# Optimization experiments

Hardware: AMD Instinct MI355X
Metric: run time of the kernel (lower is better)

## Reference

```python
import jax, jax.numpy as jnp
import numpy as np

B, C, H, W, HEADS = 8, 256, 64, 64, 4
EPS = 1e-5  # torch InstanceNorm2d default eps


def conv1x1(x, w):
    # w: [out_c, in_c]; x: [b, in_c, h, w]
    return jnp.einsum('oc,bchw->bohw', w, x)


def maxpool2(x):
    b, c, h, w = x.shape
    return x.reshape(b, c, h // 2, 2, w // 2, 2).max(axis=(3, 5))


def inorm_affine(x, g, b):
    # InstanceNorm2d(affine=True): normalize per (batch, channel) over H,W
    m = jnp.mean(x, axis=(2, 3), keepdims=True)
    v = jnp.mean((x - m) ** 2, axis=(2, 3), keepdims=True)
    return (x - m) * jax.lax.rsqrt(v + EPS) * g[None, :, None, None] + b[None, :, None, None]


def setup_inputs() -> dict:
    key = jax.random.key(0)
    ks = jax.random.split(key, 12)
    s = 1.0 / np.sqrt(C)  # fan-in style scaling for 1x1 conv weights
    return {
        'x': jax.random.normal(ks[0], (B, C, H, W), jnp.float32),
        'theta_w': jax.random.normal(ks[1], (C, C), jnp.float32) * s,
        'phi_w': jax.random.normal(ks[2], (C, C), jnp.float32) * s,
        'g_w': jax.random.normal(ks[3], (C // 2, C), jnp.float32) * s,
        'o_w': jax.random.normal(ks[4], (C, C // 2), jnp.float32) * np.sqrt(2.0 / C),
        'nt_w': 1.0 + 0.1 * jax.random.normal(ks[5], (C,), jnp.float32),
        'nt_b': 0.1 * jax.random.normal(ks[6], (C,), jnp.float32),
        'np_w': 1.0 + 0.1 * jax.random.normal(ks[7], (C,), jnp.float32),
        'np_b': 0.1 * jax.random.normal(ks[8], (C,), jnp.float32),
        'ng_w': 1.0 + 0.1 * jax.random.normal(ks[9], (C // 2,), jnp.float32),
        'ng_b': 0.1 * jax.random.normal(ks[10], (C // 2,), jnp.float32),
        'gamma': jnp.float32(0.5),
    }


def reference(x, theta_w, phi_w, g_w, o_w, nt_w, nt_b, np_w, np_b, ng_w, ng_b, gamma):
    b, c, h, w = x.shape
    n = h * w            # query length
    m = n // 4           # key/value length after 2x2 maxpool
    theta = inorm_affine(conv1x1(x, theta_w), nt_w, nt_b)
    phi = inorm_affine(maxpool2(conv1x1(x, phi_w)), np_w, np_b)
    g = inorm_affine(maxpool2(conv1x1(x, g_w)), ng_w, ng_b)
    # custom head layout: channel dim split as (C//heads, heads), head dim INNER
    theta_ = theta.reshape(b, c // HEADS, HEADS, n)
    phi_ = phi.reshape(b, c // HEADS, HEADS, m)
    g_ = g.reshape(b, (c // 2) // HEADS, HEADS, m)
    beta = jax.nn.softmax(jnp.einsum('bchi,bchj->bhij', theta_, phi_), axis=-1)
    o = jnp.einsum('bchj,bhij->bchi', g_, beta).reshape(b, c // 2, h, w)
    o = conv1x1(o, o_w)
    return gamma * o + x
```

## Files before the change

### kernel.cpp

```cpp
#include <hip/hip_runtime.h>
#include <hip/hip_bf16.h>
#include <math.h>

typedef float f32x4 __attribute__((ext_vector_type(4)));
typedef float f32x16 __attribute__((ext_vector_type(16)));
typedef __bf16 b16x8 __attribute__((ext_vector_type(8)));
typedef __bf16 b16x4 __attribute__((ext_vector_type(4)));
typedef unsigned int u32x2 __attribute__((ext_vector_type(2)));
typedef unsigned int u32x4 __attribute__((ext_vector_type(4)));

#define L2E 1.44269504088896340736f

__global__ void prep_weights(const float* tw, const float* pw, const float* gw,
                             const float* ow, __bf16* Wp, __bf16* OWp) {
    int idx = blockIdx.x * 256 + threadIdx.x;
    if (idx < 640 * 256) {
        int m = idx >> 8, k = idx & 255;
        float v;
        if (m < 256)      { int o = ((m & 63) << 2) + (m >> 6);            v = tw[o * 256 + k]; }
        else if (m < 512) { int mm = m - 256; int o = ((mm & 63) << 2) + (mm >> 6); v = pw[o * 256 + k]; }
        else              { int mm = m - 512; int o = ((mm & 31) << 2) + (mm >> 5); v = gw[o * 256 + k]; }
        Wp[idx] = (__bf16)v;
    } else {
        int j = idx - 640 * 256;
        if (j < 256 * 128) {
            int m = j >> 7, c = j & 127;
            int o = ((c & 31) << 2) + (c >> 5);
            OWp[j] = (__bf16)ow[m * 128 + o];
        }
    }
}

__global__ void transpose_x(const float* x, __bf16* xt) {
    __shared__ float tile[32][33];
    int b = blockIdx.z, c0 = blockIdx.y * 32, p0 = blockIdx.x * 32;
    int tx = threadIdx.x & 31, ty = threadIdx.x >> 5;
#pragma unroll
    for (int i = 0; i < 4; i++) {
        int cy = ty + i * 8;
        tile[cy][tx] = x[((size_t)(b * 256 + c0 + cy)) * 4096 + p0 + tx];
    }
    __syncthreads();
#pragma unroll
    for (int i = 0; i < 4; i++) {
        int py = ty + i * 8;
        xt[((size_t)b * 4096 + p0 + py) * 256 + c0 + tx] = (__bf16)tile[tx][py];
    }
}

__global__ __launch_bounds__(256) void conv_gemm(const __bf16* __restrict__ Wp,
                                                 const __bf16* __restrict__ xt,
                                                 __bf16* theta_t, __bf16* phi_t, __bf16* g_t) {
    int b = blockIdx.z, mt = blockIdx.y, nt = blockIdx.x;
    __shared__ __bf16 Al[128 * 40];
    __shared__ __bf16 Bl[128 * 40];
    int tid = threadIdx.x, l = tid & 63, w = tid >> 6;
    int wm = w >> 1, wn = w & 1, lr = l & 15, lg = l >> 4;
    f32x4 acc[4][4];
#pragma unroll
    for (int i = 0; i < 4; i++)
#pragma unroll
        for (int j = 0; j < 4; j++)
#pragma unroll
            for (int r = 0; r < 4; r++) acc[i][j][r] = 0.f;
    const __bf16* Ag = Wp + (size_t)mt * 128 * 256;
    const __bf16* Bg = xt + ((size_t)b * 4096 + nt * 128) * 256;
    int srow = tid >> 2, scol = (tid & 3) * 8;
    b16x8 aR[2], bR[2];
#pragma unroll
    for (int hh = 0; hh < 2; hh++) {
        int r = srow + hh * 64;
        aR[hh] = *(const b16x8*)&Ag[(size_t)r * 256 + scol];
        bR[hh] = *(const b16x8*)&Bg[(size_t)r * 256 + scol];
    }
    for (int k0 = 0; k0 < 256; k0 += 32) {
        if (k0) __syncthreads();
#pragma unroll
        for (int hh = 0; hh < 2; hh++) {
            int r = srow + hh * 64;
            *(b16x8*)&Al[r * 40 + scol] = aR[hh];
            *(b16x8*)&Bl[r * 40 + scol] = bR[hh];
        }
        __syncthreads();
        if (k0 < 224) {
#pragma unroll
            for (int hh = 0; hh < 2; hh++) {
                int r = srow + hh * 64;
                aR[hh] = *(const b16x8*)&Ag[(size_t)r * 256 + k0 + 32 + scol];
                bR[hh] = *(const b16x8*)&Bg[(size_t)r * 256 + k0 + 32 + scol];
            }
        }
        int ko = lg * 8;
        b16x8 af[4], bfr[4];
#pragma unroll
        for (int i = 0; i < 4; i++) af[i]  = *(b16x8*)&Al[(wm * 64 + i * 16 + lr) * 40 + ko];
#pragma unroll
        for (int i = 0; i < 4; i++) bfr[i] = *(b16x8*)&Bl[(wn * 64 + i * 16 + lr) * 40 + ko];
#pragma unroll
        for (int i = 0; i < 4; i++)
#pragma unroll
            for (int j = 0; j < 4; j++)
                acc[i][j] = __builtin_amdgcn_mfma_f32_16x16x32_bf16(af[i], bfr[j], acc[i][j], 0, 0, 0);
    }
    int rbase = lg * 4;
#pragma unroll
    for (int i = 0; i < 4; i++) {
        int m = mt * 128 + wm * 64 + i * 16 + rbase;
#pragma unroll
        for (int j = 0; j < 4; j++) {
            int p = nt * 128 + wn * 64 + j * 16 + lr;
            b16x4 v;
#pragma unroll
            for (int r = 0; r < 4; r++) v[r] = (__bf16)acc[i][j][r];
            if (m < 256)      *(b16x4*)&theta_t[((size_t)b * 4096 + p) * 256 + m] = v;
            else if (m < 512) *(b16x4*)&phi_t[((size_t)b * 4096 + p) * 256 + (m - 256)] = v;
            else              *(b16x4*)&g_t[((size_t)b * 4096 + p) * 128 + (m - 512)] = v;
        }
    }
}

__global__ __launch_bounds__(256) void theta_stats(const __bf16* __restrict__ src,
                                                   float* p1, float* p2) {
    __shared__ float S1[8][256], S2[8][256];
    int b = blockIdx.y, blk = blockIdx.x;
    int tid = threadIdx.x, cg = tid & 31, rg = tid >> 5;
    float a1[8], a2[8];
#pragma unroll
    for (int e = 0; e < 8; e++) { a1[e] = 0.f; a2[e] = 0.f; }
    const __bf16* base = src + ((size_t)b * 4096 + blk * 64 + rg * 8) * 256 + cg * 8;
#pragma unroll
    for (int r = 0; r < 8; r++) {
        b16x8 v = *(const b16x8*)&base[(size_t)r * 256];
#pragma unroll
        for (int e = 0; e < 8; e++) { float f = (float)v[e]; a1[e] += f; a2[e] += f * f; }
    }
#pragma unroll
    for (int e = 0; e < 8; e++) { S1[rg][cg * 8 + e] = a1[e]; S2[rg][cg * 8 + e] = a2[e]; }
    __syncthreads();
    float s1 = 0.f, s2 = 0.f;
#pragma unroll
    for (int i = 0; i < 8; i++) { s1 += S1[i][tid]; s2 += S2[i][tid]; }
    p1[(b * 64 + blk) * 256 + tid] = s1;
    p2[(b * 64 + blk) * 256 + tid] = s2;
}

__global__ __launch_bounds__(256) void pool_phi(const __bf16* __restrict__ src, __bf16* dst,
                                                float* p1, float* p2) {
    __shared__ float S1[8][256], S2[8][256];
    int b = blockIdx.y, qc = blockIdx.x;
    int tid = threadIdx.x, cg = tid & 31, qg = tid >> 5;
    float a1[8], a2[8];
#pragma unroll
    for (int e = 0; e < 8; e++) { a1[e] = 0.f; a2[e] = 0.f; }
#pragma unroll
    for (int qq = 0; qq < 4; qq++) {
        int q = qc * 32 + qg * 4 + qq, qy = q >> 5, qx = q & 31;
        size_t base = ((size_t)(b * 4096) + qy * 128 + qx * 2) * 256 + cg * 8;
        b16x8 v0 = *(const b16x8*)&src[base];
        b16x8 v1 = *(const b16x8*)&src[base + 256];
        b16x8 v2 = *(const b16x8*)&src[base + 16384];
        b16x8 v3 = *(const b16x8*)&src[base + 16640];
        b16x8 mv;
#pragma unroll
        for (int e = 0; e < 8; e++) {
            float m = fmaxf(fmaxf((float)v0[e], (float)v1[e]), fmaxf((float)v2[e], (float)v3[e]));
            mv[e] = (__bf16)m; a1[e] += m; a2[e] += m * m;
        }
        *(b16x8*)&dst[((size_t)b * 1024 + q) * 256 + cg * 8] = mv;
    }
#pragma unroll
    for (int e = 0; e < 8; e++) { S1[qg][cg * 8 + e] = a1[e]; S2[qg][cg * 8 + e] = a2[e]; }
    __syncthreads();
    float s1 = 0.f, s2 = 0.f;
#pragma unroll
    for (int i = 0; i < 8; i++) { s1 += S1[i][tid]; s2 += S2[i][tid]; }
    p1[(b * 32 + qc) * 256 + tid] = s1;
    p2[(b * 32 + qc) * 256 + tid] = s2;
}

__global__ __launch_bounds__(256) void pool_gT(const __bf16* __restrict__ src, __bf16* gT,
                                               float* p1, float* p2) {
    __shared__ __bf16 Pt[64][136];
    __shared__ float S1[16][128], S2[16][128];
    int b = blockIdx.y, qc = blockIdx.x;
    int tid = threadIdx.x, cg = tid & 15, qg = tid >> 4;
    float a1[8], a2[8];
#pragma unroll
    for (int e = 0; e < 8; e++) { a1[e] = 0.f; a2[e] = 0.f; }
#pragma unroll
    for (int qq = 0; qq < 4; qq++) {
        int ql = qg * 4 + qq, q = qc * 64 + ql;
        int qy = q >> 5, qx = q & 31;
        size_t base = ((size_t)(b * 4096) + qy * 128 + qx * 2) * 128 + cg * 8;
        b16x8 v0 = *(const b16x8*)&src[base];
        b16x8 v1 = *(const b16x8*)&src[base + 128];
        b16x8 v2 = *(const b16x8*)&src[base + 8192];
        b16x8 v3 = *(const b16x8*)&src[base + 8320];
        b16x8 mv;
#pragma unroll
        for (int e = 0; e < 8; e++) {
            float m = fmaxf(fmaxf((float)v0[e], (float)v1[e]), fmaxf((float)v2[e], (float)v3[e]));
            mv[e] = (__bf16)m; a1[e] += m; a2[e] += m * m;
        }
        *(b16x8*)&Pt[ql][cg * 8] = mv;
    }
#pragma unroll
    for (int e = 0; e < 8; e++) { S1[qg][cg * 8 + e] = a1[e]; S2[qg][cg * 8 + e] = a2[e]; }
    __syncthreads();
    if (tid < 128) {
        float s1 = 0.f, s2 = 0.f;
#pragma unroll
        for (int i = 0; i < 16; i++) { s1 += S1[i][tid]; s2 += S2[i][tid]; }
        p1[(b * 16 + qc) * 128 + tid] = s1;
        p2[(b * 16 + qc) * 128 + tid] = s2;
    }
    int c = tid & 127, qh = tid >> 7;
    int hh = c >> 5, ch = c & 31;
#pragma unroll
    for (int sg = 0; sg < 4; sg++) {
        int seg = qh * 4 + sg;
        b16x8 v;
#pragma unroll
        for (int e = 0; e < 8; e++) v[e] = Pt[seg * 8 + e][c];
        *(b16x8*)&gT[((((size_t)(b * 4 + hh) * 16 + qc) * 8 + seg) * 32 + ch) * 8] = v;
    }
}

__global__ void finalize_stats(const float* tp1, const float* tp2, const float* pp1,
                               const float* pp2, const float* gp1, const float* gp2,
                               const float* ntw, const float* ntb, const float* npw,
                               const float* npb, const float* ngw, const float* ngb,
                               float* sct, float* bit, float* scp, float* bip,
                               float* scg, float* big) {
    int idx = blockIdx.x * 256 + threadIdx.x;
    if (idx >= 8 * 640) return;
    int b = idx / 640, c = idx % 640;
    if (c < 256) {
        float s1 = 0.f, s2 = 0.f;
        for (int i = 0; i < 64; i++) { s1 += tp1[(b * 64 + i) * 256 + c]; s2 += tp2[(b * 64 + i) * 256 + c]; }
        float n = 4096.f;
        float m = s1 / n, v = s2 / n - m * m;
        float r = rsqrtf(v + 1e-5f);
        int o = ((c & 63) << 2) + (c >> 6);
        float wv = ntw[o], bv = ntb[o];
        sct[b * 256 + c] = r * wv * L2E;
        bit[b * 256 + c] = (bv - m * r * wv) * L2E;
    } else if (c < 512) {
        int cc = c - 256;
        float s1 = 0.f, s2 = 0.f;
        for (int i = 0; i < 32; i++) { s1 += pp1[(b * 32 + i) * 256 + cc]; s2 += pp2[(b * 32 + i) * 256 + cc]; }
        float n = 1024.f;
        float m = s1 / n, v = s2 / n - m * m;
        float r = rsqrtf(v + 1e-5f);
        int o = ((cc & 63) << 2) + (cc >> 6);
        float wv = npw[o], bv = npb[o];
        scp[b * 256 + cc] = r * wv; bip[b * 256 + cc] = bv - m * r * wv;
    } else {
        int cc = c - 512;
        float s1 = 0.f, s2 = 0.f;
        for (int i = 0; i < 16; i++) { s1 += gp1[(b * 16 + i) * 128 + cc]; s2 += gp2[(b * 16 + i) * 128 + cc]; }
        float n = 1024.f;
        float m = s1 / n, v = s2 / n - m * m;
        float r = rsqrtf(v + 1e-5f);
        int o = ((cc & 31) << 2) + (cc >> 5);
        float wv = ngw[o], bv = ngb[o];
        scg[b * 128 + cc] = r * wv; big[b * 128 + cc] = bv - m * r * wv;
    }
}

__global__ void normalize_phi(const __bf16* __restrict__ php, __bf16* __restrict__ phk,
                              const float* __restrict__ scp, const float* __restrict__ bip) {
    int blk = blockIdx.x, t = threadIdx.x;
    int b = blk >> 6, h = (blk >> 4) & 3, cc = blk & 15;
#pragma unroll
    for (int uu = 0; uu < 2; uu++) {
        int u = uu * 256 + t;
        int slot = u >> 6, key = u & 63;
        int q = cc * 64 + key;
        int cfull = h * 64 + (slot >> 1) * 16 + (slot & 1) * 8;
        b16x8 v = *(const b16x8*)&php[((size_t)b * 1024 + q) * 256 + cfull];
        b16x8 nv;
#pragma unroll
        for (int e = 0; e < 8; e++)
            nv[e] = (__bf16)((float)v[e] * scp[b * 256 + cfull + e] + bip[b * 256 + cfull + e]);
        *(b16x8*)&phk[((((size_t)(b * 4 + h) * 16 + cc) * 8 + slot) * 64 + key) * 8] = nv;
    }
}

__global__ __launch_bounds__(256, 2) void attn(const __bf16* __restrict__ theta_t,
                                               const __bf16* __restrict__ phk,
                                               const __bf16* __restrict__ gTz,
                                               const float* __restrict__ sct,
                                               const float* __restrict__ bit,
                                               const float* __restrict__ scg,
                                               const float* __restrict__ big,
                                               __bf16* __restrict__ o_mid) {
    __shared__ float comb[2][64][34];
    int bid = blockIdx.x;
    int idx = bid >> 3;
    int bh = (bid & 7) * 4 + (idx >> 5), qt = idx & 31;
    int b = bh >> 2, h = bh & 3;
    int tid = threadIdx.x, w = tid >> 6, lane = tid & 63;
    int l31 = lane & 31, hi = lane >> 5;
    int wq = w >> 1, wk = w & 1;
    int qb = qt * 128 + wq * 64;

    b16x8 qf[2][4];
#pragma unroll
    for (int m = 0; m < 2; m++) {
        int q = qb + m * 32 + l31;
        const __bf16* qp = theta_t + ((size_t)b * 4096 + q) * 256 + h * 64;
#pragma unroll
        for (int st = 0; st < 4; st++) {
            int cb = st * 16 + hi * 8;
            b16x8 raw = *(const b16x8*)&qp[cb];
            b16x8 nv;
#pragma unroll
            for (int e = 0; e < 8; e++) {
                int cix = b * 256 + h * 64 + cb + e;
                nv[e] = (__bf16)((float)raw[e] * sct[cix] + bit[cix]);
            }
            qf[m][st] = nv;
        }
    }

    const __bf16* Kg = phk + (size_t)bh * 65536 + (size_t)hi * 512 + (size_t)l31 * 8;
    const __bf16* Vg = gTz + (size_t)bh * 32768 + (size_t)hi * 256 + (size_t)l31 * 8;

    f32x16 oacc[2];
    float l_run[2] = {0.f, 0.f};
#pragma unroll
    for (int m = 0; m < 2; m++)
#pragma unroll
        for (int r = 0; r < 16; r++) oacc[m][r] = 0.f;
    f32x16 zc;
#pragma unroll
    for (int r = 0; r < 16; r++) zc[r] = 0.f;

    b16x8 akA[2][4], avA[4], akB[2][4], avB[4];

#define LOADK(dst, c) { _Pragma("unroll") for (int kf = 0; kf < 2; kf++) \
    _Pragma("unroll") for (int st = 0; st < 4; st++) \
        dst[kf][st] = *(const b16x8*)&Kg[(size_t)(c) * 4096 + st * 1024 + kf * 256]; }
#define LOADV(dst, c) { _Pragma("unroll") for (int js = 0; js < 4; js++) \
    dst[js] = *(const b16x8*)&Vg[(size_t)(c) * 2048 + js * 512]; }
#define COMPUTE(ak, av) { \
    _Pragma("unroll") for (int m = 0; m < 2; m++) { \
        _Pragma("unroll") for (int kf = 0; kf < 2; kf++) { \
            __builtin_amdgcn_s_setprio(1); \
            f32x16 s = __builtin_amdgcn_mfma_f32_32x32x16_bf16(ak[kf][0], qf[m][0], zc, 0, 0, 0); \
            _Pragma("unroll") for (int st = 1; st < 4; st++) \
                s = __builtin_amdgcn_mfma_f32_32x32x16_bf16(ak[kf][st], qf[m][st], s, 0, 0, 0); \
            __builtin_amdgcn_s_setprio(0); \
            float s0 = 0.f, s1 = 0.f, s2p = 0.f, s3 = 0.f; \
            _Pragma("unroll") for (int r = 0; r < 16; r += 4) { \
                float p0 = __builtin_amdgcn_exp2f(s[r]); \
                float p1 = __builtin_amdgcn_exp2f(s[r + 1]); \
                float p2 = __builtin_amdgcn_exp2f(s[r + 2]); \
                float p3 = __builtin_amdgcn_exp2f(s[r + 3]); \
                s[r] = p0; s[r + 1] = p1; s[r + 2] = p2; s[r + 3] = p3; \
                s0 += p0; s1 += p1; s2p += p2; s3 += p3; \
            } \
            l_run[m] += (s0 + s1) + (s2p + s3); \
            _Pragma("unroll") for (int hh2 = 0; hh2 < 2; hh2++) { \
                b16x4 A4, B4; \
                _Pragma("unroll") for (int e = 0; e < 4; e++) { \
                    A4[e] = (__bf16)s[hh2 * 8 + e]; B4[e] = (__bf16)s[hh2 * 8 + 4 + e]; } \
                u32x2 a2 = __builtin_bit_cast(u32x2, A4); \
                u32x2 b2 = __builtin_bit_cast(u32x2, B4); \
                u32x2 q0 = __builtin_amdgcn_permlane32_swap(a2[0], b2[0], false, false); \
                u32x2 q1 = __builtin_amdgcn_permlane32_swap(a2[1], b2[1], false, false); \
                u32x4 pd = {q0[0], q1[0], q0[1], q1[1]}; \
                b16x8 pf = __builtin_bit_cast(b16x8, pd); \
                __builtin_amdgcn_s_setprio(1); \
                oacc[m] = __builtin_amdgcn_mfma_f32_32x32x16_bf16(av[kf * 2 + hh2], pf, oacc[m], 0, 0, 0); \
                __builtin_amdgcn_s_setprio(0); \
            } \
        } \
    } }

    int c0 = wk * 8;
    LOADK(akA, c0) LOADV(avA, c0)
#pragma unroll 1
    for (int cc = 0; cc < 8; cc += 2) {
        int c = c0 + cc;
        LOADK(akB, c + 1) LOADV(avB, c + 1)
        COMPUTE(akA, avA)
        if (cc + 2 < 8) { LOADK(akA, c + 2) LOADV(avA, c + 2) }
        COMPUTE(akB, avB)
    }
#undef LOADK
#undef LOADV
#undef COMPUTE

    if (wk == 1) {
#pragma unroll
        for (int r = 0; r < 16; r++) {
            comb[wq][lane][r] = oacc[0][r];
            comb[wq][lane][16 + r] = oacc[1][r];
        }
        comb[wq][lane][32] = l_run[0];
        comb[wq][lane][33] = l_run[1];
    }
    __syncthreads();
    if (wk == 0) {
#pragma unroll
        for (int r = 0; r < 16; r++) {
            oacc[0][r] += comb[wq][lane][r];
            oacc[1][r] += comb[wq][lane][16 + r];
        }
        l_run[0] += comb[wq][lane][32];
        l_run[1] += comb[wq][lane][33];
#pragma unroll
        for (int m = 0; m < 2; m++) {
            float lr = l_run[m] + __shfl_xor(l_run[m], 32, 64);
            float rl = 1.0f / lr;
            int q = qb + m * 32 + l31;
#pragma unroll
            for (int rr = 0; rr < 4; rr++) {
                b16x4 v;
#pragma unroll
                for (int e = 0; e < 4; e++) {
                    int ci = b * 128 + h * 32 + rr * 8 + hi * 4 + e;
                    v[e] = (__bf16)(oacc[m][rr * 4 + e] * rl * scg[ci] + big[ci]);
                }
                *(b16x4*)&o_mid[((size_t)b * 4096 + q) * 128 + h * 32 + rr * 8 + hi * 4] = v;
            }
        }
    }
}

__global__ __launch_bounds__(256) void out_gemm(const __bf16* __restrict__ OWp,
                                                const __bf16* __restrict__ o_mid,
                                                const float* __restrict__ x,
                                                const float* gamma, float* out) {
    int b = blockIdx.z, mt = blockIdx.y, nt = blockIdx.x;
    __shared__ __bf16 Al[128 * 40];
    __shared__ __bf16 Bl[128 * 40];
    int tid = threadIdx.x, l = tid & 63, w = tid >> 6;
    int wm = w >> 1, wn = w & 1, lr = l & 15, lg = l >> 4;
    f32x4 acc[4][4];
#pragma unroll
    for (int i = 0; i < 4; i++)
#pragma unroll
        for (int j = 0; j < 4; j++)
#pragma unroll
            for (int r = 0; r < 4; r++) acc[i][j][r] = 0.f;
    const __bf16* Ag = OWp + (size_t)mt * 128 * 128;
    const __bf16* Bg = o_mid + ((size_t)b * 4096 + nt * 128) * 128;
    int srow = tid >> 2, scol = (tid & 3) * 8;
    b16x8 aR[2], bR[2];
#pragma unroll
    for (int hh = 0; hh < 2; hh++) {
        int r = srow + hh * 64;
        aR[hh] = *(const b16x8*)&Ag[(size_t)r * 128 + scol];
        bR[hh] = *(const b16x8*)&Bg[(size_t)r * 128 + scol];
    }
    for (int k0 = 0; k0 < 128; k0 += 32) {
        if (k0) __syncthreads();
#pragma unroll
        for (int hh = 0; hh < 2; hh++) {
            int r = srow + hh * 64;
            *(b16x8*)&Al[r * 40 + scol] = aR[hh];
            *(b16x8*)&Bl[r * 40 + scol] = bR[hh];
        }
        __syncthreads();
        if (k0 < 96) {
#pragma unroll
            for (int hh = 0; hh < 2; hh++) {
                int r = srow + hh * 64;
                aR[hh] = *(const b16x8*)&Ag[(size_t)r * 128 + k0 + 32 + scol];
                bR[hh] = *(const b16x8*)&Bg[(size_t)r * 128 + k0 + 32 + scol];
            }
        }
        int ko = lg * 8;
        b16x8 af[4], bfr[4];
#pragma unroll
        for (int i = 0; i < 4; i++) af[i]  = *(b16x8*)&Al[(wm * 64 + i * 16 + lr) * 40 + ko];
#pragma unroll
        for (int i = 0; i < 4; i++) bfr[i] = *(b16x8*)&Bl[(wn * 64 + i * 16 + lr) * 40 + ko];
#pragma unroll
        for (int i = 0; i < 4; i++)
#pragma unroll
            for (int j = 0; j < 4; j++)
                acc[i][j] = __builtin_amdgcn_mfma_f32_16x16x32_bf16(af[i], bfr[j], acc[i][j], 0, 0, 0);
    }
    float gm = gamma[0];
    int rbase = lg * 4;
#pragma unroll
    for (int i = 0; i < 4; i++) {
        int m = mt * 128 + wm * 64 + i * 16 + rbase;
#pragma unroll
        for (int j = 0; j < 4; j++) {
            int p = nt * 128 + wn * 64 + j * 16 + lr;
#pragma unroll
            for (int r = 0; r < 4; r++) {
                size_t o = ((size_t)b * 256 + m + r) * 4096 + p;
                out[o] = gm * acc[i][j][r] + x[o];
            }
        }
    }
}

extern "C" void kernel_launch(void* const* d_in, const int* in_sizes, int n_in,
                              void* d_out, int out_size, void* d_ws, size_t ws_size,
                              hipStream_t stream) {
    const float* x   = (const float*)d_in[0];
    const float* tw  = (const float*)d_in[1];
    const float* pw  = (const float*)d_in[2];
    const float* gw  = (const float*)d_in[3];
    const float* ow  = (const float*)d_in[4];
    const float* ntw = (const float*)d_in[5];
    const float* ntb = (const float*)d_in[6];
    const float* npw = (const float*)d_in[7];
    const float* npb = (const float*)d_in[8];
    const float* ngw = (const float*)d_in[9];
    const float* ngb = (const float*)d_in[10];
    const float* gamma = (const float*)d_in[11];
    float* out = (float*)d_out;
    char* ws = (char*)d_ws;

    __bf16* Wp  = (__bf16*)(ws + 0);
    __bf16* OWp = (__bf16*)(ws + 327680);
    __bf16* xt  = (__bf16*)(ws + 393216);
    __bf16* th  = (__bf16*)(ws + 17170432);
    __bf16* phr = (__bf16*)(ws + 33947648);
    __bf16* ghr = (__bf16*)(ws + 50724864);
    __bf16* php = (__bf16*)(ws + 59113472);
    __bf16* gT  = (__bf16*)(ws + 63307776);
    float* sb   = (float*)(ws + 65445888);

    float* tp1 = (float*)(ws + 393216);
    float* tp2 = (float*)(ws + 917504);
    float* pp1 = (float*)(ws + 1441792);
    float* pp2 = (float*)(ws + 1703936);
    float* gp1 = (float*)(ws + 1966080);
    float* gp2 = (float*)(ws + 2031616);
    __bf16* phk = phr;
    __bf16* om  = xt;

    float *sct = sb, *bit = sb + 2048, *scp = sb + 4096, *bip = sb + 6144,
          *scg = sb + 8192, *big = sb + 9216;

    prep_weights<<<768, 256, 0, stream>>>(tw, pw, gw, ow, Wp, OWp);
    transpose_x<<<dim3(128, 8, 8), 256, 0, stream>>>(x, xt);
    conv_gemm<<<dim3(32, 5, 8), 256, 0, stream>>>(Wp, xt, th, phr, ghr);
    theta_stats<<<dim3(64, 8), 256, 0, stream>>>(th, tp1, tp2);
    pool_phi<<<dim3(32, 8), 256, 0, stream>>>(phr, php, pp1, pp2);
    pool_gT<<<dim3(16, 8), 256, 0, stream>>>(ghr, gT, gp1, gp2);
    finalize_stats<<<20, 256, 0, stream>>>(tp1, tp2, pp1, pp2, gp1, gp2,
                                           ntw, ntb, npw, npb, ngw, ngb,
                                           sct, bit, scp, bip, scg, big);
    normalize_phi<<<512, 256, 0, stream>>>(php, phk, scp, bip);
    attn<<<1024, 256, 0, stream>>>(th, phk, gT, sct, bit, scg, big, om);
    out_gemm<<<dim3(32, 2, 8), 256, 0, stream>>>(OWp, om, x, gamma, out);
}
```

Baseline: 126.7 us.

## Stage K/V tiles in LDS via async global_load_lds, drop split-K combine

The attention kernel now loads each K/V chunk cooperatively into double-buffered shared memory with global_load_lds. All four waves read it from LDS, so each wave no longer fetches its own copy from global memory. Each wave now owns 64 queries across all 16 key chunks, which removes the two-wave key split and its shared-memory combine step, and the grid is halved to 512 blocks. The costs are a block-wide barrier per chunk, less parallelism across the grid, and the loss of the s_setprio hints.

```diff
diff --git a/kernel.cpp b/kernel.cpp
--- a/kernel.cpp
+++ b/kernel.cpp
@@ -295,15 +295,15 @@
                                                const float* __restrict__ scg,
                                                const float* __restrict__ big,
                                                __bf16* __restrict__ o_mid) {
-    __shared__ float comb[2][64][34];
+    __shared__ __bf16 Kb[2][4096];
+    __shared__ __bf16 Vb[2][2048];
     int bid = blockIdx.x;
     int idx = bid >> 3;
-    int bh = (bid & 7) * 4 + (idx >> 5), qt = idx & 31;
+    int bh = (bid & 7) * 4 + (idx >> 4), qt = idx & 15;
     int b = bh >> 2, h = bh & 3;
     int tid = threadIdx.x, w = tid >> 6, lane = tid & 63;
     int l31 = lane & 31, hi = lane >> 5;
-    int wq = w >> 1, wk = w & 1;
-    int qb = qt * 128 + wq * 64;
+    int qb = qt * 256 + w * 64;
 
     b16x8 qf[2][4];
 #pragma unroll
@@ -324,8 +324,8 @@
         }
     }
 
-    const __bf16* Kg = phk + (size_t)bh * 65536 + (size_t)hi * 512 + (size_t)l31 * 8;
-    const __bf16* Vg = gTz + (size_t)bh * 32768 + (size_t)hi * 256 + (size_t)l31 * 8;
+    const __bf16* Kg = phk + (size_t)bh * 65536;
+    const __bf16* Vg = gTz + (size_t)bh * 32768;
 
     f32x16 oacc[2];
     float l_run[2] = {0.f, 0.f};
@@ -337,21 +337,29 @@
 #pragma unroll
     for (int r = 0; r < 16; r++) zc[r] = 0.f;
 
-    b16x8 akA[2][4], avA[4], akB[2][4], avB[4];
-
-#define LOADK(dst, c) { _Pragma("unroll") for (int kf = 0; kf < 2; kf++) \
+#define ISSUE(buf, cc) { \
+    __builtin_amdgcn_global_load_lds( \
+        (const __attribute__((address_space(1))) void*)(Kg + (size_t)(cc) * 4096 + (w * 2) * 512 + lane * 8), \
+        (__attribute__((address_space(3))) void*)(&Kb[buf][(w * 2) * 512]), 16, 0, 0); \
+    __builtin_amdgcn_global_load_lds( \
+        (const __attribute__((address_space(1))) void*)(Kg + (size_t)(cc) * 4096 + (w * 2 + 1) * 512 + lane * 8), \
+        (__attribute__((address_space(3))) void*)(&Kb[buf][(w * 2 + 1) * 512]), 16, 0, 0); \
+    __builtin_amdgcn_global_load_lds( \
+        (const __attribute__((address_space(1))) void*)(Vg + (size_t)(cc) * 2048 + w * 512 + lane * 8), \
+        (__attribute__((address_space(3))) void*)(&Vb[buf][w * 512]), 16, 0, 0); }
+
+#define COMPUTE(cur) { \
+    b16x8 ak[2][4], av[4]; \
+    _Pragma("unroll") for (int kf = 0; kf < 2; kf++) \
     _Pragma("unroll") for (int st = 0; st < 4; st++) \
-        dst[kf][st] = *(const b16x8*)&Kg[(size_t)(c) * 4096 + st * 1024 + kf * 256]; }
-#define LOADV(dst, c) { _Pragma("unroll") for (int js = 0; js < 4; js++) \
-    dst[js] = *(const b16x8*)&Vg[(size_t)(c) * 2048 + js * 512]; }
-#define COMPUTE(ak, av) { \
+        ak[kf][st] = *(b16x8*)&Kb[cur][(st * 2 + hi) * 512 + (kf * 32 + l31) * 8]; \
+    _Pragma("unroll") for (int js = 0; js < 4; js++) \
+        av[js] = *(b16x8*)&Vb[cur][((js * 2 + hi) * 32 + l31) * 8]; \
     _Pragma("unroll") for (int m = 0; m < 2; m++) { \
         _Pragma("unroll") for (int kf = 0; kf < 2; kf++) { \
-            __builtin_amdgcn_s_setprio(1); \
             f32x16 s = __builtin_amdgcn_mfma_f32_32x32x16_bf16(ak[kf][0], qf[m][0], zc, 0, 0, 0); \
             _Pragma("unroll") for (int st = 1; st < 4; st++) \
                 s = __builtin_amdgcn_mfma_f32_32x32x16_bf16(ak[kf][st], qf[m][st], s, 0, 0, 0); \
-            __builtin_amdgcn_s_setprio(0); \
             float s0 = 0.f, s1 = 0.f, s2p = 0.f, s3 = 0.f; \
             _Pragma("unroll") for (int r = 0; r < 16; r += 4) { \
                 float p0 = __builtin_amdgcn_exp2f(s[r]); \
@@ -372,60 +380,36 @@
                 u32x2 q1 = __builtin_amdgcn_permlane32_swap(a2[1], b2[1], false, false); \
                 u32x4 pd = {q0[0], q1[0], q0[1], q1[1]}; \
                 b16x8 pf = __builtin_bit_cast(b16x8, pd); \
-                __builtin_amdgcn_s_setprio(1); \
                 oacc[m] = __builtin_amdgcn_mfma_f32_32x32x16_bf16(av[kf * 2 + hh2], pf, oacc[m], 0, 0, 0); \
-                __builtin_amdgcn_s_setprio(0); \
             } \
         } \
     } }
 
-    int c0 = wk * 8;
-    LOADK(akA, c0) LOADV(avA, c0)
+    ISSUE(0, 0)
+    __syncthreads();
 #pragma unroll 1
-    for (int cc = 0; cc < 8; cc += 2) {
-        int c = c0 + cc;
-        LOADK(akB, c + 1) LOADV(avB, c + 1)
-        COMPUTE(akA, avA)
-        if (cc + 2 < 8) { LOADK(akA, c + 2) LOADV(avA, c + 2) }
-        COMPUTE(akB, avB)
-    }
-#undef LOADK
-#undef LOADV
+    for (int c = 0; c < 16; c++) {
+        if (c < 15) ISSUE((c + 1) & 1, c + 1)
+        COMPUTE(c & 1)
+        __syncthreads();
+    }
+#undef ISSUE
 #undef COMPUTE
 
-    if (wk == 1) {
-#pragma unroll
-        for (int r = 0; r < 16; r++) {
-            comb[wq][lane][r] = oacc[0][r];
-            comb[wq][lane][16 + r] = oacc[1][r];
-        }
-        comb[wq][lane][32] = l_run[0];
-        comb[wq][lane][33] = l_run[1];
-    }
-    __syncthreads();
-    if (wk == 0) {
-#pragma unroll
-        for (int r = 0; r < 16; r++) {
-            oacc[0][r] += comb[wq][lane][r];
-            oacc[1][r] += comb[wq][lane][16 + r];
-        }
-        l_run[0] += comb[wq][lane][32];
-        l_run[1] += comb[wq][lane][33];
-#pragma unroll
-        for (int m = 0; m < 2; m++) {
-            float lr = l_run[m] + __shfl_xor(l_run[m], 32, 64);
-            float rl = 1.0f / lr;
-            int q = qb + m * 32 + l31;
-#pragma unroll
-            for (int rr = 0; rr < 4; rr++) {
-                b16x4 v;
-#pragma unroll
-                for (int e = 0; e < 4; e++) {
-                    int ci = b * 128 + h * 32 + rr * 8 + hi * 4 + e;
-                    v[e] = (__bf16)(oacc[m][rr * 4 + e] * rl * scg[ci] + big[ci]);
-                }
-                *(b16x4*)&o_mid[((size_t)b * 4096 + q) * 128 + h * 32 + rr * 8 + hi * 4] = v;
+#pragma unroll
+    for (int m = 0; m < 2; m++) {
+        float lr = l_run[m] + __shfl_xor(l_run[m], 32, 64);
+        float rl = 1.0f / lr;
+        int q = qb + m * 32 + l31;
+#pragma unroll
+        for (int rr = 0; rr < 4; rr++) {
+            b16x4 v;
+#pragma unroll
+            for (int e = 0; e < 4; e++) {
+                int ci = b * 128 + h * 32 + rr * 8 + hi * 4 + e;
+                v[e] = (__bf16)(oacc[m][rr * 4 + e] * rl * scg[ci] + big[ci]);
             }
+            *(b16x4*)&o_mid[((size_t)b * 4096 + q) * 128 + h * 32 + rr * 8 + hi * 4] = v;
         }
     }
 }
@@ -552,6 +536,6 @@
                                            ntw, ntb, npw, npb, ngw, ngb,
                                            sct, bit, scp, bip, scg, big);
     normalize_phi<<<512, 256, 0, stream>>>(php, phk, scp, bip);
-    attn<<<1024, 256, 0, stream>>>(th, phk, gT, sct, bit, scg, big, om);
+    attn<<<512, 256, 0, stream>>>(th, phk, gT, sct, bit, scg, big, om);
     out_gemm<<<dim3(32, 2, 8), 256, 0, stream>>>(OWp, om, x, gamma, out);
 }
```

After: 124.5 us. Within noise of the previous version (-1.7%).
